# Performance work log

Hardware: AMD Instinct MI355X
Metric: run time of the kernel (lower is better)

## Reference

```python
import jax, jax.numpy as jnp
import numpy as np

N = 204800   # total nodes (4096 subgraphs x 50 nodes)
E = 3276800  # edges (avg degree 16)
B = 4096     # number of subgraphs
IN = 64      # in_feats
HID = 32     # latent_dim per layer
CAT = 128    # 4 * 32 concatenated states
PH = 64      # pooling hidden dim
R = 3        # num_relations
NB = 2       # num_bases
MARGIN = 1.0


def setup_inputs() -> dict:
    key = jax.random.key(0)
    ks = jax.random.split(key, 24)
    s = 0.1
    inp = {}
    inp['x'] = jax.random.normal(ks[0], (N, IN), jnp.float32)
    inp['edge_norm'] = jax.random.uniform(ks[1], (E,), jnp.float32)
    inp['src'] = jax.random.randint(ks[2], (E,), 0, N, jnp.int32)
    inp['dst'] = jax.random.randint(ks[3], (E,), 0, N, jnp.int32)
    inp['etype'] = jax.random.randint(ks[4], (E,), 0, R, jnp.int32)
    inp['graph_id'] = jnp.arange(N, dtype=jnp.int32) // (N // B)
    inp['ntype'] = jax.random.randint(ks[5], (N,), 0, 2, jnp.int32)
    # layer 0: basis-decomposed RelGraphConv (in=64 -> 32)
    inp['bases0'] = jax.random.normal(ks[6], (NB, IN, HID), jnp.float32) * s
    inp['coef0'] = jax.random.normal(ks[7], (R, NB), jnp.float32)
    inp['wself0'] = jax.random.normal(ks[8], (IN, HID), jnp.float32) * s
    inp['bias0'] = jnp.zeros((HID,), jnp.float32)
    # layers 1..3 stacked (32 -> 32 each)
    inp['bases_r'] = jax.random.normal(ks[9], (3, NB, HID, HID), jnp.float32) * s
    inp['coef_r'] = jax.random.normal(ks[10], (3, R, NB), jnp.float32)
    inp['wself_r'] = jax.random.normal(ks[11], (3, HID, HID), jnp.float32) * s
    inp['bias_r'] = jnp.zeros((3, HID), jnp.float32)
    # attention pooling (user / item)
    inp['wp_u'] = jax.random.normal(ks[12], (CAT, PH), jnp.float32) * s
    inp['wt_u'] = jax.random.normal(ks[13], (CAT, PH), jnp.float32) * s
    inp['wp_i'] = jax.random.normal(ks[14], (CAT, PH), jnp.float32) * s
    inp['wt_i'] = jax.random.normal(ks[15], (CAT, PH), jnp.float32) * s
    # MLP head
    inp['w1'] = jax.random.normal(ks[16], (2 * PH, 64), jnp.float32) * s
    inp['b1'] = jnp.zeros((64,), jnp.float32)
    inp['w2'] = jax.random.normal(ks[17], (64, 1), jnp.float32) * s
    inp['b2'] = jnp.zeros((1,), jnp.float32)
    return inp


def _rgcn_layer(h, bases, coef, wself, bias, src, dst, etype, edge_norm):
    # basis decomposition: W_r = sum_b coef[r,b] * bases[b]
    W = jnp.einsum('rb,bio->rio', coef, bases)          # [R, in, out]
    xr = jnp.einsum('ni,rio->nro', h, W)                # [N, R, out] (transform then gather)
    msg = xr[src, etype] * edge_norm[:, None]           # [E, out]
    agg = jax.ops.segment_sum(msg, dst, num_segments=N) # scatter-add to dst
    return jnp.tanh(agg + h @ wself + bias)


def _attn_pool(x, mask, gid, wp, wt):
    # x: [N, CAT], mask: [N] bool (target node type), gid: [N] graph ids
    fmask = mask.astype(x.dtype)
    cnt = jax.ops.segment_sum(fmask, gid, num_segments=B)              # [B]
    tmean = jax.ops.segment_sum(x * fmask[:, None], gid, num_segments=B)
    tmean = tmean / (cnt[:, None] + 1e-8)                              # [B, CAT]
    p = x @ wp                                                          # [N, PH]
    t = tmean @ wt                                                      # [B, PH]
    score = jnp.sum(p * t[gid], axis=-1) / jnp.sqrt(jnp.float32(PH))    # [N]
    score = jnp.where(mask, score, -1e9)
    m = jax.ops.segment_max(score, gid, num_segments=B)                 # [B]
    a = jnp.exp(score - m[gid]) * fmask
    z = jax.ops.segment_sum(a, gid, num_segments=B)
    alpha = a / (z[gid] + 1e-8)
    return jax.ops.segment_sum(alpha[:, None] * p, gid, num_segments=B)  # [B, PH]


def reference(x, edge_norm, src, dst, etype, graph_id, ntype,
              bases0, coef0, wself0, bias0, bases_r, coef_r, wself_r, bias_r,
              wp_u, wt_u, wp_i, wt_i, w1, b1, w2, b2):
    h = x
    states = []
    h = _rgcn_layer(h, bases0, coef0, wself0, bias0, src, dst, etype, edge_norm)
    states.append(h)
    for l in range(3):
        h = _rgcn_layer(h, bases_r[l], coef_r[l], wself_r[l], bias_r[l],
                        src, dst, etype, edge_norm)
        states.append(h)
    hcat = jnp.concatenate(states, axis=1)  # [N, 128]

    mask_u = ntype == 0
    mask_i = ntype == 1

    # triplet contrastive loss over per-graph mean user/item embeddings
    fu = mask_u.astype(hcat.dtype)
    fi = mask_i.astype(hcat.dtype)
    cu = jax.ops.segment_sum(fu, graph_id, num_segments=B) + 1e-8
    ci = jax.ops.segment_sum(fi, graph_id, num_segments=B) + 1e-8
    au = jax.ops.segment_sum(hcat * fu[:, None], graph_id, num_segments=B) / cu[:, None]
    ai = jax.ops.segment_sum(hcat * fi[:, None], graph_id, num_segments=B) / ci[:, None]
    an = jnp.roll(ai, 1, axis=0)  # negatives from shifted graphs
    dpos = jnp.sum((au - ai) ** 2, axis=-1)
    dneg = jnp.sum((au - an) ** 2, axis=-1)
    triplet_loss = jnp.mean(jax.nn.relu(dpos - dneg + MARGIN))

    x_u = _attn_pool(hcat, mask_u, graph_id, wp_u, wt_u)  # [B, 64]
    x_i = _attn_pool(hcat, mask_i, graph_id, wp_i, wt_i)  # [B, 64]
    z = jnp.concatenate([x_u, x_i], axis=1)               # [B, 128]
    z = jax.nn.relu(z @ w1 + b1)                          # dropout off (eval)
    out = jax.nn.sigmoid(z @ w2 + b2)[:, 0]               # [B]
    return out, triplet_loss
```

## Files before the change

### kernel.cpp

```cpp
#include <hip/hip_runtime.h>
#include <cstdint>
#include <cstddef>

#define NN   204800
#define EE   3276800
#define BB   4096
#define GS   50
#define NBUCK 200
#define CHUNK 8192
#define BCAP  17408

typedef __attribute__((ext_vector_type(8))) short short8v;
typedef __attribute__((ext_vector_type(4))) float f32x4;

__device__ __forceinline__ float bf2f(unsigned short u) {
  unsigned int x = ((unsigned int)u) << 16;
  return __int_as_float((int)x);
}
__device__ __forceinline__ unsigned short f2bf(float f) {
  unsigned int x = __float_as_uint(f);
  unsigned int r = (x + 0x7fffu + ((x >> 16) & 1u)) >> 16;
  return (unsigned short)r;
}

__global__ __launch_bounds__(256) void init_cursor_kernel(int* __restrict__ gcursor) {
  const int t = threadIdx.x;
  if (t < NBUCK) gcursor[t] = t * BCAP;
}

__global__ __launch_bounds__(256) void pass1_kernel(const int* __restrict__ src,
                                                    const int* __restrict__ dst,
                                                    const int* __restrict__ etype,
                                                    const float* __restrict__ en,
                                                    int* __restrict__ gcursor,
                                                    int2* __restrict__ staging) {
  __shared__ int2 stage[CHUNK];
  __shared__ unsigned char bid[CHUNK];
  __shared__ int hist[NBUCK], cur[NBUCK], lo[NBUCK], gbase[NBUCK];
  __shared__ int sc[256];
  const int tid = threadIdx.x;
  const int ebase = blockIdx.x * CHUNK;

  for (int i = tid; i < NBUCK; i += 256) hist[i] = 0;
  __syncthreads();
  for (int i = tid; i < CHUNK; i += 256) {
    int bk = dst[ebase + i] >> 10;
    bid[i] = (unsigned char)bk;
    atomicAdd(&hist[bk], 1);
  }
  __syncthreads();
  int hv = (tid < NBUCK) ? hist[tid] : 0;
  sc[tid] = hv;
  __syncthreads();
  for (int off = 1; off < 256; off <<= 1) {
    int t = (tid >= off) ? sc[tid - off] : 0;
    __syncthreads();
    sc[tid] += t;
    __syncthreads();
  }
  if (tid < NBUCK) {
    int excl = sc[tid] - hv;
    lo[tid]  = excl;
    cur[tid] = excl;
    gbase[tid] = hv ? atomicAdd(&gcursor[tid], hv) : 0;
  }
  __syncthreads();
  for (int i = tid; i < CHUNK; i += 256) {
    int bk = bid[i];
    int p = atomicAdd(&cur[bk], 1);
    int s  = src[ebase + i];
    int et = etype[ebase + i];
    int d  = dst[ebase + i];
    int2 r;
    r.x = (s << 12) | (et << 10) | (d & 1023);
    r.y = __float_as_int(en[ebase + i]);
    stage[p] = r;
  }
  __syncthreads();
  const int wave = tid >> 6, lane = tid & 63;
  for (int bk = wave; bk < NBUCK; bk += 4) {
    const int len = hist[bk];
    const int l0  = lo[bk];
    const int gb  = gbase[bk];
    for (int i = lane; i < len; i += 64)
      staging[gb + i] = stage[l0 + i];
  }
}

__global__ __launch_bounds__(256) void pass2_kernel(const int2* __restrict__ staging,
                                                    const int* __restrict__ gcursor,
                                                    int* __restrict__ begs,
                                                    int* __restrict__ ends,
                                                    int2* __restrict__ edata) {
  __shared__ int lhist[1024];
  __shared__ int lcur[1024];
  __shared__ int psum[256];
  const int b = blockIdx.x;
  const int tid = threadIdx.x;
  const int base = b * BCAP;
  const int cnt  = gcursor[b] - base;

  for (int i = tid; i < 1024; i += 256) lhist[i] = 0;
  __syncthreads();
  for (int i = tid; i < cnt; i += 256)
    atomicAdd(&lhist[staging[base + i].x & 1023], 1);
  __syncthreads();
  int s0 = lhist[4 * tid], s1 = lhist[4 * tid + 1];
  int s2 = lhist[4 * tid + 2], s3 = lhist[4 * tid + 3];
  int tot = s0 + s1 + s2 + s3;
  psum[tid] = tot;
  __syncthreads();
  for (int off = 1; off < 256; off <<= 1) {
    int t = (tid >= off) ? psum[tid - off] : 0;
    __syncthreads();
    psum[tid] += t;
    __syncthreads();
  }
  int o0 = base + psum[tid] - tot;
  int o1 = o0 + s0, o2 = o1 + s1, o3 = o2 + s2;
  const int nodeb = b * 1024;
  begs[nodeb + 4 * tid]     = o0;  ends[nodeb + 4 * tid]     = o1;  lcur[4 * tid]     = o0;
  begs[nodeb + 4 * tid + 1] = o1;  ends[nodeb + 4 * tid + 1] = o2;  lcur[4 * tid + 1] = o1;
  begs[nodeb + 4 * tid + 2] = o2;  ends[nodeb + 4 * tid + 2] = o3;  lcur[4 * tid + 2] = o2;
  begs[nodeb + 4 * tid + 3] = o3;  ends[nodeb + 4 * tid + 3] = o3 + s3;  lcur[4 * tid + 3] = o3;
  __syncthreads();
  for (int i = tid; i < cnt; i += 256) {
    int2 r = staging[base + i];
    int pos = atomicAdd(&lcur[r.x & 1023], 1);
    int s  = r.x >> 12;
    int et = (r.x >> 10) & 3;
    int2 outr;
    outr.x = s * 192 + et * 64;
    outr.y = r.y;
    edata[pos] = outr;
  }
}

__global__ __launch_bounds__(256) void wprep_kernel(
    const float* __restrict__ bases0, const float* __restrict__ coef0,
    const float* __restrict__ wself0,
    const float* __restrict__ bases_r, const float* __restrict__ coef_r,
    const float* __restrict__ wself_r,
    const float* __restrict__ wp_u, const float* __restrict__ wp_i,
    const float* __restrict__ wt_u, const float* __restrict__ wt_i,
    const float* __restrict__ w1,
    float* __restrict__ Wbuf) {
  int idx = blockIdx.x * 256 + threadIdx.x;
  if (idx < 8192) {
    int i = idx >> 7, j = idx & 127;
    float v;
    if (j < 96) {
      int r = j >> 5, f = j & 31;
      v = coef0[r * 2 + 0] * bases0[0 * 2048 + i * 32 + f]
        + coef0[r * 2 + 1] * bases0[1 * 2048 + i * 32 + f];
    } else {
      v = wself0[i * 32 + (j - 96)];
    }
    Wbuf[idx] = v;
    return;
  }
  int idx2 = idx - 8192;
  if (idx2 < 3 * 4096) {
    int l = idx2 >> 12, rem = idx2 & 4095;
    int i = rem >> 7, j = rem & 127;
    float v;
    if (j < 96) {
      int r = j >> 5, f = j & 31;
      v = coef_r[l * 6 + r * 2 + 0] * bases_r[l * 2048 + 0 * 1024 + i * 32 + f]
        + coef_r[l * 6 + r * 2 + 1] * bases_r[l * 2048 + 1 * 1024 + i * 32 + f];
    } else {
      v = wself_r[l * 1024 + i * 32 + (j - 96)];
    }
    Wbuf[idx] = v;
    return;
  }
  int idx3 = idx2 - 12288;
  if (idx3 < 32768) {
    int side = idx3 >> 14;
    int r = idx3 & 16383;
    int kk = r >> 7, k = r & 127;
    const float* wp = side ? wp_i : wp_u;
    const float* wt = side ? wt_i : wt_u;
    float acc = 0.f;
#pragma unroll 8
    for (int j = 0; j < 64; ++j)
      acc = fmaf(wp[k * 64 + j], wt[kk * 64 + j], acc);
    Wbuf[idx] = acc * 0.125f;
    return;
  }
  int idx4 = idx3 - 32768;
  if (idx4 < 16384) {
    int kp = idx4 >> 6, t = idx4 & 63;
    int side = kp >> 7, k = kp & 127;
    const float* wp = side ? wp_i : wp_u;
    float acc = 0.f;
#pragma unroll 8
    for (int j = 0; j < 64; ++j)
      acc = fmaf(wp[k * 64 + j], w1[(side * 64 + j) * 64 + t], acc);
    Wbuf[idx] = acc;
  }
}

__global__ __launch_bounds__(256) void wprep2_kernel(const float* __restrict__ Wbuf,
                                                     unsigned short* __restrict__ Whi,
                                                     unsigned short* __restrict__ Wlo) {
  int e = blockIdx.x * 256 + threadIdx.x;
  if (e >= 20480) return;
  float v;
  if (e < 8192) {
    int j = e & 7, l = (e >> 3) & 63, c = (e >> 9) & 7, q = e >> 12;
    int k   = q * 32 + (l >> 4) * 8 + j;
    int col = c * 16 + (l & 15);
    v = Wbuf[k * 128 + col];
  } else {
    int e2 = e - 8192;
    int lay = e2 >> 12, r = e2 & 4095;
    int j = r & 7, l = (r >> 3) & 63, c = r >> 9;
    int k   = (l >> 4) * 8 + j;
    int col = c * 16 + (l & 15);
    v = Wbuf[8192 + lay * 4096 + k * 128 + col];
  }
  unsigned short hi = f2bf(v);
  Whi[e] = hi;
  Wlo[e] = f2bf(v - bf2f(hi));
}

__global__ __launch_bounds__(256) void cvt_bf16_kernel(const float* __restrict__ in,
                                                       unsigned short* __restrict__ hi,
                                                       unsigned short* __restrict__ lo,
                                                       int n4) {
  int i = blockIdx.x * 256 + threadIdx.x;
  if (i < n4) {
    const float4 a = reinterpret_cast<const float4*>(in)[i];
    ushort4 h, l;
    h.x = f2bf(a.x); l.x = f2bf(a.x - bf2f(h.x));
    h.y = f2bf(a.y); l.y = f2bf(a.y - bf2f(h.y));
    h.z = f2bf(a.z); l.z = f2bf(a.z - bf2f(h.z));
    h.w = f2bf(a.w); l.w = f2bf(a.w - bf2f(h.w));
    reinterpret_cast<ushort4*>(hi)[i] = h;
    reinterpret_cast<ushort4*>(lo)[i] = l;
  }
}

template <int K, bool ALO>
__global__ __launch_bounds__(256) void transform_mfma_kernel(
    const unsigned short* __restrict__ Ahi, const unsigned short* __restrict__ Alo,
    const unsigned short* __restrict__ Whi, const unsigned short* __restrict__ Wlo,
    unsigned short* __restrict__ Tb, float* __restrict__ Sf) {
  __shared__ float C[64][129];
  const int tid = threadIdx.x;
  const int wv = tid >> 6, l = tid & 63;
  const int l15 = l & 15, kg = l >> 4;
  const int row = blockIdx.x * 64 + wv * 16 + l15;

  short8v ah[K / 32], al[K / 32];
#pragma unroll
  for (int q = 0; q < K / 32; ++q) {
    ah[q] = *reinterpret_cast<const short8v*>(Ahi + (size_t)row * K + q * 32 + kg * 8);
    if (ALO)
      al[q] = *reinterpret_cast<const short8v*>(Alo + (size_t)row * K + q * 32 + kg * 8);
  }

#pragma unroll
  for (int c = 0; c < 8; ++c) {
    f32x4 a = {0.f, 0.f, 0.f, 0.f};
#pragma unroll
    for (int q = 0; q < K / 32; ++q) {
      const size_t fb = ((size_t)(q * 8 + c) * 64 + l) * 8;
      const short8v bh = *reinterpret_cast<const short8v*>(Whi + fb);
      const short8v bl = *reinterpret_cast<const short8v*>(Wlo + fb);
      a = __builtin_amdgcn_mfma_f32_16x16x32_bf16(ah[q], bh, a, 0, 0, 0);
      if (ALO)
        a = __builtin_amdgcn_mfma_f32_16x16x32_bf16(al[q], bh, a, 0, 0, 0);
      a = __builtin_amdgcn_mfma_f32_16x16x32_bf16(ah[q], bl, a, 0, 0, 0);
    }
#pragma unroll
    for (int r = 0; r < 4; ++r)
      C[wv * 16 + kg * 4 + r][c * 16 + l15] = a[r];
  }
  __syncthreads();

  const int row64 = tid & 63, q = tid >> 6;
  const int node = blockIdx.x * 64 + row64;
  if (q < 3) {
#pragma unroll
    for (int v = 0; v < 4; ++v) {
      const int cb = q * 32 + v * 8;
      uint4 pk;
      pk.x = (unsigned)f2bf(C[row64][cb + 0]) | ((unsigned)f2bf(C[row64][cb + 1]) << 16);
      pk.y = (unsigned)f2bf(C[row64][cb + 2]) | ((unsigned)f2bf(C[row64][cb + 3]) << 16);
      pk.z = (unsigned)f2bf(C[row64][cb + 4]) | ((unsigned)f2bf(C[row64][cb + 5]) << 16);
      pk.w = (unsigned)f2bf(C[row64][cb + 6]) | ((unsigned)f2bf(C[row64][cb + 7]) << 16);
      *reinterpret_cast<uint4*>(Tb + (size_t)node * 96 + cb) = pk;
    }
  } else {
#pragma unroll
    for (int v = 0; v < 8; ++v) {
      float4 f;
      f.x = C[row64][96 + v * 4 + 0];
      f.y = C[row64][96 + v * 4 + 1];
      f.z = C[row64][96 + v * 4 + 2];
      f.w = C[row64][96 + v * 4 + 3];
      *reinterpret_cast<float4*>(Sf + (size_t)node * 32 + v * 4) = f;
    }
  }
}

__global__ __launch_bounds__(256) void aggregate_kernel(const unsigned short* __restrict__ Tb,
                                                        const float* __restrict__ Sf,
                                                        const int* __restrict__ begs,
                                                        const int* __restrict__ ends,
                                                        const int2* __restrict__ edata,
                                                        const float* __restrict__ bias,
                                                        float* __restrict__ hcat,
                                                        unsigned short* __restrict__ hhi,
                                                        int lslot) {
  const int node = blockIdx.x * 32 + (threadIdx.x >> 3);
  const int f4   = (threadIdx.x & 7) * 4;
  const int loff = f4 * 2;
  const char* Tbc = (const char*)Tb;
  const int beg = begs[node];
  const int end = ends[node];
  const float4 self = *reinterpret_cast<const float4*>(&Sf[(size_t)node * 32 + f4]);
  const float4 bv   = *reinterpret_cast<const float4*>(&bias[f4]);
  float ax = self.x + bv.x, ay = self.y + bv.y, az = self.z + bv.z, aw = self.w + bv.w;

  int k = beg;
  for (; k + 8 <= end; k += 8) {
    int2 ed[8];
#pragma unroll
    for (int u = 0; u < 8; ++u) ed[u] = edata[k + u];
    ushort4 mv[8];
#pragma unroll
    for (int u = 0; u < 8; ++u)
      mv[u] = *reinterpret_cast<const ushort4*>(Tbc + ed[u].x + loff);
#pragma unroll
    for (int u = 0; u < 8; ++u) {
      const float nm = __int_as_float(ed[u].y);
      ax = fmaf(bf2f(mv[u].x), nm, ax);
      ay = fmaf(bf2f(mv[u].y), nm, ay);
      az = fmaf(bf2f(mv[u].z), nm, az);
      aw = fmaf(bf2f(mv[u].w), nm, aw);
    }
  }
  for (; k < end; ++k) {
    int2 e0 = edata[k];
    const float nm = __int_as_float(e0.y);
    ushort4 m0 = *reinterpret_cast<const ushort4*>(Tbc + e0.x + loff);
    ax = fmaf(bf2f(m0.x), nm, ax);
    ay = fmaf(bf2f(m0.y), nm, ay);
    az = fmaf(bf2f(m0.z), nm, az);
    aw = fmaf(bf2f(m0.w), nm, aw);
  }
  float4 o;
  o.x = tanhf(ax); o.y = tanhf(ay); o.z = tanhf(az); o.w = tanhf(aw);
  *reinterpret_cast<float4*>(&hcat[(size_t)node * 128 + lslot * 32 + f4]) = o;
  if (hhi) {
    ushort4 h;
    h.x = f2bf(o.x); h.y = f2bf(o.y); h.z = f2bf(o.z); h.w = f2bf(o.w);
    *reinterpret_cast<ushort4*>(hhi + (size_t)node * 32 + f4) = h;
  }
}

__global__ __launch_bounds__(256) void pool_head_kernel(
    const float* __restrict__ hcat, const int* __restrict__ ntype,
    const float* __restrict__ Mt,
    const float* __restrict__ W1c,
    const float* __restrict__ b1,
    const float* __restrict__ w2, const float* __restrict__ b2,
    float* __restrict__ out, float* __restrict__ tl) {
  __shared__ float hl[GS * 129];
  __shared__ float scr[1024];
  __shared__ float av2[256];
  __shared__ float red[4];
  __shared__ float cnts[4];
  __shared__ int   snt[64];
  __shared__ int   sntp[64];

  const int g    = blockIdx.x;
  const int gp   = (g + BB - 1) & (BB - 1);
  const int tid  = threadIdx.x;
  const int lane = tid & 63;

  const float* hg  = hcat + (size_t)g  * (GS * 128);
  const float* hp  = hcat + (size_t)gp * (GS * 128);
  const int*   ntg = ntype + g  * GS;
  const int*   ntp = ntype + gp * GS;

  if (tid < 64) {
    snt[tid] = (tid < GS) ? ntg[tid] : 99;
    unsigned long long bu = __ballot(snt[tid] == 0);
    unsigned long long bi = __ballot(snt[tid] == 1);
    if (lane == 0) {
      cnts[0] = 1.f / ((float)__popcll(bu) + 1e-8f);
      cnts[1] = 1.f / ((float)__popcll(bi) + 1e-8f);
    }
  } else if (tid < 128) {
    sntp[lane] = (lane < GS) ? ntp[lane] : 99;
    unsigned long long bp = __ballot(sntp[lane] == 1);
    if (lane == 0) cnts[2] = 1.f / ((float)__popcll(bp) + 1e-8f);
  }

  {
    const int rowg = tid >> 5;
    const int kq   = (tid & 31) * 4;
    float spx = 0.f, spy = 0.f, spz = 0.f, spw = 0.f;
#pragma unroll
    for (int p = 0; p < 7; ++p) {
      const int r = rowg + 8 * p;
      if (r < GS) {
        const float4 v = *reinterpret_cast<const float4*>(hg + r * 128 + kq);
        hl[r * 129 + kq + 0] = v.x;
        hl[r * 129 + kq + 1] = v.y;
        hl[r * 129 + kq + 2] = v.z;
        hl[r * 129 + kq + 3] = v.w;
        if (ntp[r] == 1) {
          const float4 w = *reinterpret_cast<const float4*>(hp + r * 128 + kq);
          spx += w.x; spy += w.y; spz += w.z; spw += w.w;
        }
      }
    }
    scr[rowg * 128 + kq + 0] = spx;
    scr[rowg * 128 + kq + 1] = spy;
    scr[rowg * 128 + kq + 2] = spz;
    scr[rowg * 128 + kq + 3] = spw;
  }
  __syncthreads();

  if (tid < 128) {
    const int kf = tid;
    float su = 0.f, si = 0.f;
#pragma unroll
    for (int r = 0; r < GS; ++r) {
      const float v = hl[r * 129 + kf];
      if (snt[r] == 0) su += v; else si += v;
    }
    float sp = 0.f;
#pragma unroll
    for (int rg = 0; rg < 8; ++rg) sp += scr[rg * 128 + kf];
    const float auk = su * cnts[0];
    const float aik = si * cnts[1];
    const float apk = sp * cnts[2];
    av2[kf]       = auk;
    av2[128 + kf] = aik;
    float d1 = (auk - aik) * (auk - aik);
    float d2 = (auk - apk) * (auk - apk);
    for (int o = 32; o; o >>= 1) {
      d1 += __shfl_xor(d1, o);
      d2 += __shfl_xor(d2, o);
    }
    if (lane == 0) { red[tid >> 6] = d1; red[2 + (tid >> 6)] = d2; }
  }
  __syncthreads();

  {
    const int side = tid >> 7, kf = tid & 127;
    const float* M  = Mt + (size_t)side * 16384 + kf;
    const float* av = av2 + side * 128;
    float a0 = 0.f, a1 = 0.f, a2 = 0.f, a3 = 0.f;
#pragma unroll 4
    for (int kk = 0; kk < 128; kk += 4) {
      a0 = fmaf(M[(kk + 0) * 128], av[kk + 0], a0);
      a1 = fmaf(M[(kk + 1) * 128], av[kk + 1], a1);
      a2 = fmaf(M[(kk + 2) * 128], av[kk + 2], a2);
      a3 = fmaf(M[(kk + 3) * 128], av[kk + 3], a3);
    }
    scr[tid] = (a0 + a1) + (a2 + a3);
  }
  if (tid == 0) tl[g] = fmaxf(0.f, (red[0] + red[1]) - (red[2] + red[3]) + 1.0f);
  __syncthreads();

  if (tid < 128) {
    const int side = tid >> 6;
    const float* q = scr + side * 128;
    float v = -1e9f;
    bool msk = false;
    if (lane < GS) {
      msk = (snt[lane] == side);
      float a0 = 0.f, a1 = 0.f;
#pragma unroll 8
      for (int k = 0; k < 128; k += 2) {
        a0 = fmaf(hl[lane * 129 + k], q[k], a0);
        a1 = fmaf(hl[lane * 129 + k + 1], q[k + 1], a1);
      }
      v = msk ? (a0 + a1) : -1e9f;
    }
    float m = v;
    for (int o = 32; o; o >>= 1) m = fmaxf(m, __shfl_xor(m, o));
    float e = (lane < GS && msk) ? expf(v - m) : 0.f;
    float z = e;
    for (int o = 32; o; o >>= 1) z += __shfl_xor(z, o);
    const float invz = 1.f / (z + 1e-8f);
    if (lane < GS) scr[256 + side * 64 + lane] = e * invz;
  }
  __syncthreads();

  {
    const int side = tid >> 7, kf = tid & 127;
    const float* a = scr + 256 + side * 64;
    float acc = 0.f;
#pragma unroll
    for (int nl = 0; nl < GS; ++nl)
      acc = fmaf(a[nl], hl[nl * 129 + kf], acc);
    scr[384 + side * 128 + kf] = acc;
  }
  __syncthreads();

  {
    const int j = tid & 63, c = tid >> 6;
    const float* Wc = W1c + (size_t)c * 64 * 64 + j;
    const float* cv = scr + 384 + c * 64;
    float a0 = 0.f, a1 = 0.f, a2 = 0.f, a3 = 0.f;
#pragma unroll 4
    for (int k = 0; k < 64; k += 4) {
      a0 = fmaf(Wc[(k + 0) * 64], cv[k + 0], a0);
      a1 = fmaf(Wc[(k + 1) * 64], cv[k + 1], a1);
      a2 = fmaf(Wc[(k + 2) * 64], cv[k + 2], a2);
      a3 = fmaf(Wc[(k + 3) * 64], cv[k + 3], a3);
    }
    scr[640 + c * 64 + j] = (a0 + a1) + (a2 + a3);
  }
  __syncthreads();

  if (tid < 64) {
    const float z1 = fmaxf(b1[tid] + scr[640 + tid] + scr[704 + tid] +
                           scr[768 + tid] + scr[832 + tid], 0.f);
    float p = z1 * w2[tid];
    for (int o = 32; o; o >>= 1) p += __shfl_xor(p, o);
    if (tid == 0) out[g] = 1.f / (1.f + expf(-(p + b2[0])));
  }
}

__global__ __launch_bounds__(256) void tl_reduce_kernel(const float* __restrict__ tl,
                                                        float* __restrict__ out) {
  __shared__ float s[256];
  float acc = 0.f;
  for (int i = threadIdx.x; i < BB; i += 256) acc += tl[i];
  s[threadIdx.x] = acc;
  __syncthreads();
  for (int off = 128; off > 0; off >>= 1) {
    if (threadIdx.x < off) s[threadIdx.x] += s[threadIdx.x + off];
    __syncthreads();
  }
  if (threadIdx.x == 0) out[BB] = s[0] * (1.f / (float)BB);
}

extern "C" void kernel_launch(void* const* d_in, const int* in_sizes, int n_in,
                              void* d_out, int out_size, void* d_ws, size_t ws_size,
                              hipStream_t stream) {
  const float* x        = (const float*)d_in[0];
  const float* edge_nrm = (const float*)d_in[1];
  const int*   src      = (const int*)d_in[2];
  const int*   dst      = (const int*)d_in[3];
  const int*   etype    = (const int*)d_in[4];
  const int*   ntype    = (const int*)d_in[6];
  const float* bases0   = (const float*)d_in[7];
  const float* coef0    = (const float*)d_in[8];
  const float* wself0   = (const float*)d_in[9];
  const float* bias0    = (const float*)d_in[10];
  const float* bases_r  = (const float*)d_in[11];
  const float* coef_r   = (const float*)d_in[12];
  const float* wself_r  = (const float*)d_in[13];
  const float* bias_r   = (const float*)d_in[14];
  const float* wp_u     = (const float*)d_in[15];
  const float* wt_u     = (const float*)d_in[16];
  const float* wp_i     = (const float*)d_in[17];
  const float* wt_i     = (const float*)d_in[18];
  const float* w1       = (const float*)d_in[19];
  const float* b1       = (const float*)d_in[20];
  const float* w2       = (const float*)d_in[21];
  const float* b2       = (const float*)d_in[22];
  float* out = (float*)d_out;

  float*          hcat = (float*)d_ws;
  float*          R    = hcat + (size_t)NN * 128;
  int2*           staging = (int2*)R;
  unsigned short* Tb   = (unsigned short*)R;
  float*          Sf   = (float*)(Tb + (size_t)NN * 96);
  unsigned short* Ahi  = (unsigned short*)(Sf + (size_t)NN * 32);
  unsigned short* A0hi = (unsigned short*)(hcat + (size_t)NN * 64);
  unsigned short* A0lo = A0hi + (size_t)NN * 64;
  int2*  edata   = (int2*)(R + (size_t)NN * 128);
  int*   begs    = (int*)(edata + (size_t)NBUCK * BCAP);
  int*   ends    = begs + NN;
  int*   gcursor = ends + NN;
  float* Wbuf    = (float*)(gcursor + 256);
  unsigned short* Whi = (unsigned short*)(Wbuf + 69632);
  unsigned short* Wlo = Whi + 20480;
  float* tl      = Wbuf + 69632 + 10240;

  size_t need = ((size_t)NN * 128 * 2 + (size_t)NBUCK * BCAP * 2 + 2 * NN + 256 +
                 69632 + 10240 + BB) * 4;
  if (ws_size < need) return;

  init_cursor_kernel<<<1, 256, 0, stream>>>(gcursor);
  pass1_kernel<<<EE / CHUNK, 256, 0, stream>>>(src, dst, etype, edge_nrm,
                                               gcursor, staging);
  pass2_kernel<<<NBUCK, 256, 0, stream>>>(staging, gcursor, begs, ends, edata);

  wprep_kernel<<<(69632 + 255) / 256, 256, 0, stream>>>(
      bases0, coef0, wself0, bases_r, coef_r, wself_r,
      wp_u, wp_i, wt_u, wt_i, w1, Wbuf);
  wprep2_kernel<<<80, 256, 0, stream>>>(Wbuf, Whi, Wlo);
  cvt_bf16_kernel<<<(NN * 64 / 4 + 255) / 256, 256, 0, stream>>>(
      x, A0hi, A0lo, NN * 64 / 4);

  transform_mfma_kernel<64, true><<<NN / 64, 256, 0, stream>>>(
      A0hi, A0lo, Whi, Wlo, Tb, Sf);
  aggregate_kernel<<<NN / 32, 256, 0, stream>>>(Tb, Sf, begs, ends, edata, bias0,
                                                hcat, Ahi, 0);
  for (int l = 1; l <= 3; ++l) {
    transform_mfma_kernel<32, false><<<NN / 64, 256, 0, stream>>>(
        Ahi, nullptr, Whi + 8192 + (size_t)(l - 1) * 4096,
        Wlo + 8192 + (size_t)(l - 1) * 4096, Tb, Sf);
    aggregate_kernel<<<NN / 32, 256, 0, stream>>>(
        Tb, Sf, begs, ends, edata, bias_r + (l - 1) * 32, hcat,
        (l < 3) ? Ahi : (unsigned short*)nullptr, l);
  }

  pool_head_kernel<<<BB, 256, 0, stream>>>(hcat, ntype,
                                           Wbuf + 20480, Wbuf + 53248,
                                           b1, w2, b2, out, tl);
  tl_reduce_kernel<<<1, 256, 0, stream>>>(tl, out);
}
```

Measured before the change: 603.2 us.

## Aggregate raw features per relation before transform in layers 1-3

```diff
diff --git a/kernel.cpp b/kernel.cpp
--- a/kernel.cpp
+++ b/kernel.cpp
@@ -130,7 +130,7 @@
     int s  = r.x >> 12;
     int et = (r.x >> 10) & 3;
     int2 outr;
-    outr.x = s * 192 + et * 64;
+    outr.x = (s << 8) + (et << 6);
     outr.y = r.y;
     edata[pos] = outr;
   }
@@ -215,10 +215,13 @@
   } else {
     int e2 = e - 8192;
     int lay = e2 >> 12, r = e2 & 4095;
-    int j = r & 7, l = (r >> 3) & 63, c = r >> 9;
-    int k   = (l >> 4) * 8 + j;
-    int col = c * 16 + (l & 15);
-    v = Wbuf[8192 + lay * 4096 + k * 128 + col];
+    int j = r & 7, l = (r >> 3) & 63, qc = r >> 9;
+    int q = qc >> 1, c = qc & 1;
+    int k = q * 32 + (l >> 4) * 8 + j;
+    int o = c * 16 + (l & 15);
+    const float* Wc = Wbuf + 8192 + lay * 4096;
+    v = (k < 96) ? Wc[(k & 31) * 128 + (k >> 5) * 32 + o]
+                 : Wc[(k - 96) * 128 + 96 + o];
   }
   unsigned short hi = f2bf(v);
   Whi[e] = hi;
@@ -242,36 +245,33 @@
   }
 }
 
-template <int K, bool ALO>
-__global__ __launch_bounds__(256) void transform_mfma_kernel(
+__global__ __launch_bounds__(256) void transform_l0_kernel(
     const unsigned short* __restrict__ Ahi, const unsigned short* __restrict__ Alo,
     const unsigned short* __restrict__ Whi, const unsigned short* __restrict__ Wlo,
-    unsigned short* __restrict__ Tb, float* __restrict__ Sf) {
+    unsigned short* __restrict__ Tb0) {
   __shared__ float C[64][129];
   const int tid = threadIdx.x;
   const int wv = tid >> 6, l = tid & 63;
   const int l15 = l & 15, kg = l >> 4;
   const int row = blockIdx.x * 64 + wv * 16 + l15;
 
-  short8v ah[K / 32], al[K / 32];
-#pragma unroll
-  for (int q = 0; q < K / 32; ++q) {
-    ah[q] = *reinterpret_cast<const short8v*>(Ahi + (size_t)row * K + q * 32 + kg * 8);
-    if (ALO)
-      al[q] = *reinterpret_cast<const short8v*>(Alo + (size_t)row * K + q * 32 + kg * 8);
+  short8v ah[2], al[2];
+#pragma unroll
+  for (int q = 0; q < 2; ++q) {
+    ah[q] = *reinterpret_cast<const short8v*>(Ahi + (size_t)row * 64 + q * 32 + kg * 8);
+    al[q] = *reinterpret_cast<const short8v*>(Alo + (size_t)row * 64 + q * 32 + kg * 8);
   }
 
 #pragma unroll
   for (int c = 0; c < 8; ++c) {
     f32x4 a = {0.f, 0.f, 0.f, 0.f};
 #pragma unroll
-    for (int q = 0; q < K / 32; ++q) {
+    for (int q = 0; q < 2; ++q) {
       const size_t fb = ((size_t)(q * 8 + c) * 64 + l) * 8;
       const short8v bh = *reinterpret_cast<const short8v*>(Whi + fb);
       const short8v bl = *reinterpret_cast<const short8v*>(Wlo + fb);
       a = __builtin_amdgcn_mfma_f32_16x16x32_bf16(ah[q], bh, a, 0, 0, 0);
-      if (ALO)
-        a = __builtin_amdgcn_mfma_f32_16x16x32_bf16(al[q], bh, a, 0, 0, 0);
+      a = __builtin_amdgcn_mfma_f32_16x16x32_bf16(al[q], bh, a, 0, 0, 0);
       a = __builtin_amdgcn_mfma_f32_16x16x32_bf16(ah[q], bl, a, 0, 0, 0);
     }
 #pragma unroll
@@ -282,48 +282,33 @@
 
   const int row64 = tid & 63, q = tid >> 6;
   const int node = blockIdx.x * 64 + row64;
-  if (q < 3) {
-#pragma unroll
-    for (int v = 0; v < 4; ++v) {
-      const int cb = q * 32 + v * 8;
-      uint4 pk;
-      pk.x = (unsigned)f2bf(C[row64][cb + 0]) | ((unsigned)f2bf(C[row64][cb + 1]) << 16);
-      pk.y = (unsigned)f2bf(C[row64][cb + 2]) | ((unsigned)f2bf(C[row64][cb + 3]) << 16);
-      pk.z = (unsigned)f2bf(C[row64][cb + 4]) | ((unsigned)f2bf(C[row64][cb + 5]) << 16);
-      pk.w = (unsigned)f2bf(C[row64][cb + 6]) | ((unsigned)f2bf(C[row64][cb + 7]) << 16);
-      *reinterpret_cast<uint4*>(Tb + (size_t)node * 96 + cb) = pk;
-    }
-  } else {
-#pragma unroll
-    for (int v = 0; v < 8; ++v) {
-      float4 f;
-      f.x = C[row64][96 + v * 4 + 0];
-      f.y = C[row64][96 + v * 4 + 1];
-      f.z = C[row64][96 + v * 4 + 2];
-      f.w = C[row64][96 + v * 4 + 3];
-      *reinterpret_cast<float4*>(Sf + (size_t)node * 32 + v * 4) = f;
-    }
-  }
-}
-
-__global__ __launch_bounds__(256) void aggregate_kernel(const unsigned short* __restrict__ Tb,
-                                                        const float* __restrict__ Sf,
-                                                        const int* __restrict__ begs,
-                                                        const int* __restrict__ ends,
-                                                        const int2* __restrict__ edata,
-                                                        const float* __restrict__ bias,
-                                                        float* __restrict__ hcat,
-                                                        unsigned short* __restrict__ hhi,
-                                                        int lslot) {
+#pragma unroll
+  for (int v = 0; v < 4; ++v) {
+    const int cb = q * 32 + v * 8;
+    uint4 pk;
+    pk.x = (unsigned)f2bf(C[row64][cb + 0]) | ((unsigned)f2bf(C[row64][cb + 1]) << 16);
+    pk.y = (unsigned)f2bf(C[row64][cb + 2]) | ((unsigned)f2bf(C[row64][cb + 3]) << 16);
+    pk.z = (unsigned)f2bf(C[row64][cb + 4]) | ((unsigned)f2bf(C[row64][cb + 5]) << 16);
+    pk.w = (unsigned)f2bf(C[row64][cb + 6]) | ((unsigned)f2bf(C[row64][cb + 7]) << 16);
+    *reinterpret_cast<uint4*>(Tb0 + (size_t)node * 128 + cb) = pk;
+  }
+}
+
+__global__ __launch_bounds__(256) void aggregate_l0_kernel(
+    const unsigned short* __restrict__ Tb0,
+    const int* __restrict__ begs, const int* __restrict__ ends,
+    const int2* __restrict__ edata, const float* __restrict__ bias,
+    float* __restrict__ hcat, unsigned short* __restrict__ Ab) {
   const int node = blockIdx.x * 32 + (threadIdx.x >> 3);
   const int f4   = (threadIdx.x & 7) * 4;
   const int loff = f4 * 2;
-  const char* Tbc = (const char*)Tb;
+  const char* Tbc = (const char*)Tb0;
   const int beg = begs[node];
   const int end = ends[node];
-  const float4 self = *reinterpret_cast<const float4*>(&Sf[(size_t)node * 32 + f4]);
-  const float4 bv   = *reinterpret_cast<const float4*>(&bias[f4]);
-  float ax = self.x + bv.x, ay = self.y + bv.y, az = self.z + bv.z, aw = self.w + bv.w;
+  const ushort4 sb = *reinterpret_cast<const ushort4*>(Tbc + (size_t)node * 256 + 192 + loff);
+  const float4 bv  = *reinterpret_cast<const float4*>(&bias[f4]);
+  float ax = bf2f(sb.x) + bv.x, ay = bf2f(sb.y) + bv.y;
+  float az = bf2f(sb.z) + bv.z, aw = bf2f(sb.w) + bv.w;
 
   int k = beg;
   for (; k + 8 <= end; k += 8) {
@@ -354,11 +339,128 @@
   }
   float4 o;
   o.x = tanhf(ax); o.y = tanhf(ay); o.z = tanhf(az); o.w = tanhf(aw);
-  *reinterpret_cast<float4*>(&hcat[(size_t)node * 128 + lslot * 32 + f4]) = o;
-  if (hhi) {
-    ushort4 h;
-    h.x = f2bf(o.x); h.y = f2bf(o.y); h.z = f2bf(o.z); h.w = f2bf(o.w);
-    *reinterpret_cast<ushort4*>(hhi + (size_t)node * 32 + f4) = h;
+  *reinterpret_cast<float4*>(&hcat[(size_t)node * 128 + f4]) = o;
+  ushort4 h;
+  h.x = f2bf(o.x); h.y = f2bf(o.y); h.z = f2bf(o.z); h.w = f2bf(o.w);
+  *reinterpret_cast<ushort4*>(Ab + (size_t)node * 128 + 96 + f4) = h;
+}
+
+__global__ __launch_bounds__(256) void aggregate_raw_kernel(
+    unsigned short* __restrict__ Ab,
+    const int* __restrict__ begs, const int* __restrict__ ends,
+    const int2* __restrict__ edata) {
+  const int node = blockIdx.x * 32 + (threadIdx.x >> 3);
+  const int f4   = (threadIdx.x & 7) * 4;
+  const int loff = f4 * 2;
+  const char* Abc = (const char*)Ab;
+  const int beg = begs[node];
+  const int end = ends[node];
+  float a0x = 0.f, a0y = 0.f, a0z = 0.f, a0w = 0.f;
+  float a1x = 0.f, a1y = 0.f, a1z = 0.f, a1w = 0.f;
+  float a2x = 0.f, a2y = 0.f, a2z = 0.f, a2w = 0.f;
+
+  int k = beg;
+  for (; k + 8 <= end; k += 8) {
+    int2 ed[8];
+#pragma unroll
+    for (int u = 0; u < 8; ++u) ed[u] = edata[k + u];
+    ushort4 mv[8];
+#pragma unroll
+    for (int u = 0; u < 8; ++u)
+      mv[u] = *reinterpret_cast<const ushort4*>(Abc + (ed[u].x & ~255) + 192 + loff);
+#pragma unroll
+    for (int u = 0; u < 8; ++u) {
+      const int et = (ed[u].x >> 6) & 3;
+      const float nm = __int_as_float(ed[u].y);
+      const float n0 = (et == 0) ? nm : 0.f;
+      const float n1 = (et == 1) ? nm : 0.f;
+      const float n2 = (et == 2) ? nm : 0.f;
+      const float vx = bf2f(mv[u].x), vy = bf2f(mv[u].y);
+      const float vz = bf2f(mv[u].z), vw = bf2f(mv[u].w);
+      a0x = fmaf(vx, n0, a0x); a0y = fmaf(vy, n0, a0y);
+      a0z = fmaf(vz, n0, a0z); a0w = fmaf(vw, n0, a0w);
+      a1x = fmaf(vx, n1, a1x); a1y = fmaf(vy, n1, a1y);
+      a1z = fmaf(vz, n1, a1z); a1w = fmaf(vw, n1, a1w);
+      a2x = fmaf(vx, n2, a2x); a2y = fmaf(vy, n2, a2y);
+      a2z = fmaf(vz, n2, a2z); a2w = fmaf(vw, n2, a2w);
+    }
+  }
+  for (; k < end; ++k) {
+    int2 e0 = edata[k];
+    const int et = (e0.x >> 6) & 3;
+    const float nm = __int_as_float(e0.y);
+    const float n0 = (et == 0) ? nm : 0.f;
+    const float n1 = (et == 1) ? nm : 0.f;
+    const float n2 = (et == 2) ? nm : 0.f;
+    ushort4 m0 = *reinterpret_cast<const ushort4*>(Abc + (e0.x & ~255) + 192 + loff);
+    const float vx = bf2f(m0.x), vy = bf2f(m0.y), vz = bf2f(m0.z), vw = bf2f(m0.w);
+    a0x = fmaf(vx, n0, a0x); a0y = fmaf(vy, n0, a0y);
+    a0z = fmaf(vz, n0, a0z); a0w = fmaf(vw, n0, a0w);
+    a1x = fmaf(vx, n1, a1x); a1y = fmaf(vy, n1, a1y);
+    a1z = fmaf(vz, n1, a1z); a1w = fmaf(vw, n1, a1w);
+    a2x = fmaf(vx, n2, a2x); a2y = fmaf(vy, n2, a2y);
+    a2z = fmaf(vz, n2, a2z); a2w = fmaf(vw, n2, a2w);
+  }
+  ushort4 s0, s1, s2;
+  s0.x = f2bf(a0x); s0.y = f2bf(a0y); s0.z = f2bf(a0z); s0.w = f2bf(a0w);
+  s1.x = f2bf(a1x); s1.y = f2bf(a1y); s1.z = f2bf(a1z); s1.w = f2bf(a1w);
+  s2.x = f2bf(a2x); s2.y = f2bf(a2y); s2.z = f2bf(a2z); s2.w = f2bf(a2w);
+  unsigned short* rowp = Ab + (size_t)node * 128;
+  *reinterpret_cast<ushort4*>(rowp + f4)      = s0;
+  *reinterpret_cast<ushort4*>(rowp + 32 + f4) = s1;
+  *reinterpret_cast<ushort4*>(rowp + 64 + f4) = s2;
+}
+
+__global__ __launch_bounds__(256) void transform_new_kernel(
+    const unsigned short* __restrict__ Ab,
+    const unsigned short* __restrict__ Whi, const unsigned short* __restrict__ Wlo,
+    const float* __restrict__ bias,
+    float* __restrict__ hcatSlot, unsigned short* __restrict__ AbY) {
+  __shared__ float C[64][33];
+  const int tid = threadIdx.x;
+  const int wv = tid >> 6, l = tid & 63;
+  const int l15 = l & 15, kg = l >> 4;
+  const int row = blockIdx.x * 64 + wv * 16 + l15;
+
+  short8v af[4];
+#pragma unroll
+  for (int q = 0; q < 4; ++q)
+    af[q] = *reinterpret_cast<const short8v*>(Ab + (size_t)row * 128 + q * 32 + kg * 8);
+
+#pragma unroll
+  for (int c = 0; c < 2; ++c) {
+    f32x4 a = {0.f, 0.f, 0.f, 0.f};
+#pragma unroll
+    for (int q = 0; q < 4; ++q) {
+      const size_t fb = ((size_t)(q * 2 + c) * 64 + l) * 8;
+      const short8v bh = *reinterpret_cast<const short8v*>(Whi + fb);
+      const short8v bl = *reinterpret_cast<const short8v*>(Wlo + fb);
+      a = __builtin_amdgcn_mfma_f32_16x16x32_bf16(af[q], bh, a, 0, 0, 0);
+      a = __builtin_amdgcn_mfma_f32_16x16x32_bf16(af[q], bl, a, 0, 0, 0);
+    }
+#pragma unroll
+    for (int r = 0; r < 4; ++r)
+      C[wv * 16 + kg * 4 + r][c * 16 + l15] = a[r];
+  }
+  __syncthreads();
+
+  const int row64 = tid & 63, g = tid >> 6;
+  const int node = blockIdx.x * 64 + row64;
+  float z[8];
+#pragma unroll
+  for (int v = 0; v < 8; ++v)
+    z[v] = tanhf(C[row64][g * 8 + v] + bias[g * 8 + v]);
+  float4 f0 = {z[0], z[1], z[2], z[3]};
+  float4 f1 = {z[4], z[5], z[6], z[7]};
+  *reinterpret_cast<float4*>(hcatSlot + (size_t)node * 128 + g * 8)     = f0;
+  *reinterpret_cast<float4*>(hcatSlot + (size_t)node * 128 + g * 8 + 4) = f1;
+  if (AbY) {
+    uint4 pk;
+    pk.x = (unsigned)f2bf(z[0]) | ((unsigned)f2bf(z[1]) << 16);
+    pk.y = (unsigned)f2bf(z[2]) | ((unsigned)f2bf(z[3]) << 16);
+    pk.z = (unsigned)f2bf(z[4]) | ((unsigned)f2bf(z[5]) << 16);
+    pk.w = (unsigned)f2bf(z[6]) | ((unsigned)f2bf(z[7]) << 16);
+    *reinterpret_cast<uint4*>(AbY + (size_t)node * 128 + 96 + g * 8) = pk;
   }
 }
 
@@ -377,7 +479,7 @@
   __shared__ int   snt[64];
   __shared__ int   sntp[64];
 
-  const int g    = blockIdx.x;
+  const int g    = (blockIdx.x & 7) * (BB / 8) + (blockIdx.x >> 3);
   const int gp   = (g + BB - 1) & (BB - 1);
   const int tid  = threadIdx.x;
   const int lane = tid & 63;
@@ -575,9 +677,9 @@
   float*          hcat = (float*)d_ws;
   float*          R    = hcat + (size_t)NN * 128;
   int2*           staging = (int2*)R;
-  unsigned short* Tb   = (unsigned short*)R;
-  float*          Sf   = (float*)(Tb + (size_t)NN * 96);
-  unsigned short* Ahi  = (unsigned short*)(Sf + (size_t)NN * 32);
+  unsigned short* Tb0  = (unsigned short*)R;
+  unsigned short* AbA  = Tb0 + (size_t)NN * 128;
+  unsigned short* AbB  = Tb0;
   unsigned short* A0hi = (unsigned short*)(hcat + (size_t)NN * 64);
   unsigned short* A0lo = A0hi + (size_t)NN * 64;
   int2*  edata   = (int2*)(R + (size_t)NN * 128);
@@ -605,17 +707,18 @@
   cvt_bf16_kernel<<<(NN * 64 / 4 + 255) / 256, 256, 0, stream>>>(
       x, A0hi, A0lo, NN * 64 / 4);
 
-  transform_mfma_kernel<64, true><<<NN / 64, 256, 0, stream>>>(
-      A0hi, A0lo, Whi, Wlo, Tb, Sf);
-  aggregate_kernel<<<NN / 32, 256, 0, stream>>>(Tb, Sf, begs, ends, edata, bias0,
-                                                hcat, Ahi, 0);
+  transform_l0_kernel<<<NN / 64, 256, 0, stream>>>(A0hi, A0lo, Whi, Wlo, Tb0);
+  aggregate_l0_kernel<<<NN / 32, 256, 0, stream>>>(Tb0, begs, ends, edata,
+                                                   bias0, hcat, AbA);
+
+  unsigned short* AbX[3] = {AbA, AbB, AbA};
+  unsigned short* AbY[3] = {AbB, AbA, nullptr};
   for (int l = 1; l <= 3; ++l) {
-    transform_mfma_kernel<32, false><<<NN / 64, 256, 0, stream>>>(
-        Ahi, nullptr, Whi + 8192 + (size_t)(l - 1) * 4096,
-        Wlo + 8192 + (size_t)(l - 1) * 4096, Tb, Sf);
-    aggregate_kernel<<<NN / 32, 256, 0, stream>>>(
-        Tb, Sf, begs, ends, edata, bias_r + (l - 1) * 32, hcat,
-        (l < 3) ? Ahi : (unsigned short*)nullptr, l);
+    aggregate_raw_kernel<<<NN / 32, 256, 0, stream>>>(AbX[l - 1], begs, ends, edata);
+    transform_new_kernel<<<NN / 64, 256, 0, stream>>>(
+        AbX[l - 1], Whi + 8192 + (size_t)(l - 1) * 4096,
+        Wlo + 8192 + (size_t)(l - 1) * 4096, bias_r + (l - 1) * 32,
+        hcat + (size_t)l * 32, AbY[l - 1]);
   }
 
   pool_head_kernel<<<BB, 256, 0, stream>>>(hcat, ntype,
```

Result: faster. 589.2 us (-2.3%).
